# Kernel optimization log

Hardware: AMD Instinct MI355X
Metric: run time of the kernel (lower is better)

The kernel has to match this reference:

```python
import jax, jax.numpy as jnp
import numpy as np

N_NODES = 100000
N_EDGES = 3200000
IN_CH = 256
OUT_CH = 1


def setup_inputs() -> dict:
    key = jax.random.key(0)
    ks = jax.random.split(key, 8)
    x = jax.random.normal(ks[0], (N_NODES, IN_CH), dtype=jnp.float32)
    edge_index = jax.random.randint(ks[1], (2, N_EDGES), 0, N_NODES, dtype=jnp.int64 if jax.config.jax_enable_x64 else jnp.int32)
    s_in = 1.0 / np.sqrt(IN_CH)
    Wq = jax.random.uniform(ks[2], (IN_CH, OUT_CH), jnp.float32, -s_in, s_in)
    bq = jax.random.uniform(ks[3], (OUT_CH,), jnp.float32, -s_in, s_in)
    Wk = jax.random.uniform(ks[4], (IN_CH, OUT_CH), jnp.float32, -s_in, s_in)
    bk = jax.random.uniform(ks[5], (OUT_CH,), jnp.float32, -s_in, s_in)
    Wv = jax.random.uniform(ks[6], (IN_CH, IN_CH), jnp.float32, -s_in, s_in)
    bv = jax.random.uniform(ks[7], (IN_CH,), jnp.float32, -s_in, s_in)
    return {"x": x, "edge_index": edge_index, "Wq": Wq, "bq": bq,
            "Wk": Wk, "bk": bk, "Wv": Wv, "bv": bv}


def reference(x, edge_index, Wq, bq, Wk, bk, Wv, bv):
    num_nodes = x.shape[0]
    q = x @ Wq + bq                       # [N, out_ch]
    k = x @ Wk + bk                       # [N, out_ch]
    v = x @ Wv + bv                       # [N, in_ch]
    row, col = edge_index[0], edge_index[1]
    # edge attention logits: gather + dot over out_ch
    att = jnp.sum(q[row] * k[col], axis=-1)          # [E]
    att = jax.nn.leaky_relu(att, negative_slope=0.2)
    att = jax.nn.softmax(att, axis=0)                # softmax over ALL edges (dim=0)
    # scatter-add edge attention to source nodes
    attention_weights = jax.ops.segment_sum(att, row, num_segments=num_nodes)  # [N]
    graph_emb = jnp.sum(attention_weights[:, None] * v, axis=0)                # [in_ch]
    return graph_emb, attention_weights
```

## Files before the change

### kernel.cpp

```cpp
#include <hip/hip_runtime.h>

#define N_NODES 100000
#define N_EDGES 3200000
#define CH 256

#define EPB 2048
#define GS 1563
#define NB2 25
#define BSZ 4096
#define G_AGG 16
#define SLICE 98
#define GRID_QK 1563
#define GRID_POOL 512

#define OFF_TOTAL  0
#define OFF_PTOT   16
#define OFF_YUP    1584
#define OFF_PRE    132656
#define OFF_Q      173296
#define OFF_K      273296
#define OFF_PART   373296
#define OFF_EX     2011696
#define OFF_ROW    5212720

__global__ __launch_bounds__(256) void k_qk(const float* __restrict__ x,
                                            const float* __restrict__ Wq,
                                            const float* __restrict__ bq,
                                            const float* __restrict__ Wk,
                                            const float* __restrict__ bk,
                                            float* __restrict__ q,
                                            float* __restrict__ k) {
    int t = threadIdx.x;
    int w = t >> 6, lane = t & 63;
    int g = lane >> 4, seg = lane & 15;
    float4 wq4[4], wk4[4];
    #pragma unroll
    for (int j = 0; j < 4; ++j) {
        wq4[j] = ((const float4*)Wq)[seg + 16 * j];
        wk4[j] = ((const float4*)Wk)[seg + 16 * j];
    }
    float bqs = bq[0], bks = bk[0];
    int base = blockIdx.x * 64 + w * 16 + g;
    #pragma unroll
    for (int i = 0; i < 4; ++i) {
        int n = base + i * 4;
        if (n < N_NODES) {
            const float4* xr = (const float4*)(x + (size_t)n * CH);
            float dq = 0.0f, dk = 0.0f;
            #pragma unroll
            for (int j = 0; j < 4; ++j) {
                float4 xv = xr[seg + 16 * j];
                dq = fmaf(xv.x, wq4[j].x, fmaf(xv.y, wq4[j].y,
                     fmaf(xv.z, wq4[j].z, fmaf(xv.w, wq4[j].w, dq))));
                dk = fmaf(xv.x, wk4[j].x, fmaf(xv.y, wk4[j].y,
                     fmaf(xv.z, wk4[j].z, fmaf(xv.w, wk4[j].w, dk))));
            }
            dq += __shfl_down(dq, 8); dq += __shfl_down(dq, 4);
            dq += __shfl_down(dq, 2); dq += __shfl_down(dq, 1);
            dk += __shfl_down(dk, 8); dk += __shfl_down(dk, 4);
            dk += __shfl_down(dk, 2); dk += __shfl_down(dk, 1);
            if (seg == 0) { q[n] = dq + bqs; k[n] = dk + bks; }
        }
    }
}

__global__ __launch_bounds__(256) void k_sort(const int* __restrict__ ei,
                                              const float* __restrict__ q,
                                              const float* __restrict__ k,
                                              float* __restrict__ ex_out,
                                              unsigned short* __restrict__ row_out,
                                              int* __restrict__ pre,
                                              float* __restrict__ ptot) {
    __shared__ int cnt[4][NB2];
    __shared__ int bsum[NB2];
    __shared__ int pref[NB2 + 1];
    __shared__ float lex[EPB];
    __shared__ unsigned short lrow[EPB];
    __shared__ float sm[4];
    int t = threadIdx.x, blk = blockIdx.x, w = t >> 6;
    int e0 = blk * EPB;
    int ecnt = min(EPB, N_EDGES - e0);
    if (t < 4 * NB2) ((int*)cnt)[t] = 0;
    __syncthreads();
    int rr[8]; float ee[8];
    #pragma unroll
    for (int j = 0; j < 8; ++j) {
        int i = j * 256 + t;
        if (i < ecnt) {
            int r = ei[e0 + i], c = ei[N_EDGES + e0 + i];
            float v = q[r] * k[c];
            v = (v >= 0.0f) ? v : 0.2f * v;
            rr[j] = r; ee[j] = __expf(v);
            atomicAdd(&cnt[w][r >> 12], 1);
        } else { rr[j] = -1; ee[j] = 0.0f; }
    }
    __syncthreads();
    if (t < NB2) {
        int c0 = cnt[0][t], c1 = cnt[1][t], c2 = cnt[2][t], c3 = cnt[3][t];
        cnt[0][t] = 0; cnt[1][t] = c0; cnt[2][t] = c0 + c1; cnt[3][t] = c0 + c1 + c2;
        bsum[t] = c0 + c1 + c2 + c3;
    }
    __syncthreads();
    if (t == 0) {
        int run = 0;
        #pragma unroll
        for (int b = 0; b < NB2; ++b) { pref[b] = run; run += bsum[b]; }
        pref[NB2] = run;
    }
    __syncthreads();
    if (t < 4 * NB2) { int ww = t / NB2, b = t - ww * NB2; cnt[ww][b] += pref[b]; }
    if (t < NB2 + 1) pre[blk * 26 + t] = pref[t];
    __syncthreads();
    #pragma unroll
    for (int j = 0; j < 8; ++j) {
        if (rr[j] >= 0) {
            int b = rr[j] >> 12;
            int p = atomicAdd(&cnt[w][b], 1);
            lex[p] = ee[j];
            lrow[p] = (unsigned short)(rr[j] & (BSZ - 1));
        }
    }
    float s = ((ee[0] + ee[1]) + (ee[2] + ee[3])) + ((ee[4] + ee[5]) + (ee[6] + ee[7]));
    #pragma unroll
    for (int off = 32; off; off >>= 1) s += __shfl_down(s, off);
    if ((t & 63) == 0) sm[w] = s;
    __syncthreads();
    if (t == 0) ptot[blk] = sm[0] + sm[1] + sm[2] + sm[3];
    size_t gb = (size_t)blk * EPB;
    for (int i = t; i < ecnt; i += 256) ex_out[gb + i] = lex[i];
    unsigned* ro = (unsigned*)(row_out + gb);
    const unsigned* lr = (const unsigned*)lrow;
    int words = (ecnt + 1) >> 1;
    for (int i = t; i < words; i += 256) ro[i] = lr[i];
}

__global__ __launch_bounds__(256) void k_agg(const float* __restrict__ ex,
                                             const unsigned short* __restrict__ row,
                                             const int* __restrict__ pre,
                                             float* __restrict__ partial) {
    int b = blockIdx.x / G_AGG, g = blockIdx.x % G_AGG;
    __shared__ float acc[BSZ];
    int t = threadIdx.x, w = t >> 6, lane = t & 63;
    for (int i = t; i < BSZ; i += 256) acc[i] = 0.0f;
    __syncthreads();
    int sb0 = g * SLICE, sb1 = min(sb0 + SLICE, GS);
    for (int sb = sb0 + w; sb < sb1; sb += 4) {
        size_t gbase = (size_t)sb * EPB;
        int s0 = pre[sb * 26 + b], s1 = pre[sb * 26 + b + 1];
        for (int i = s0 + lane; i < s1; i += 64)
            atomicAdd(&acc[row[gbase + i]], ex[gbase + i]);
    }
    __syncthreads();
    float* dst = partial + ((size_t)b * G_AGG + g) * BSZ;
    for (int i = t; i < BSZ; i += 256) dst[i] = acc[i];
}

__global__ __launch_bounds__(256) void k_pool(const float* __restrict__ x,
                                              const float* __restrict__ partial,
                                              const float* __restrict__ ptot,
                                              float* __restrict__ totalp,
                                              float* __restrict__ yup,
                                              float* __restrict__ aw_out) {
    int t = threadIdx.x, s = t >> 6, g = t & 63;
    float ts = 0.0f;
    for (int i = t; i < GS; i += 256) ts += ptot[i];
    #pragma unroll
    for (int off = 32; off; off >>= 1) ts += __shfl_down(ts, off);
    __shared__ float sm[4];
    __shared__ float totsh;
    if (g == 0) sm[s] = ts;
    __syncthreads();
    if (t == 0) {
        totsh = sm[0] + sm[1] + sm[2] + sm[3];
        if (blockIdx.x == 0) totalp[0] = totsh;
    }
    __syncthreads();
    float inv = 1.0f / totsh;

    __shared__ float awA[2][8], awB[2][8];
    const float4* X4 = (const float4*)x;
    float4 acc = make_float4(0.f, 0.f, 0.f, 0.f);
    int p = 0;
    for (int base = blockIdx.x * 8; base < N_NODES; base += GRID_POOL * 8, p ^= 1) {
        int bkt = base >> 12, off = base & (BSZ - 1);
        float pv = 0.0f;
        if (t < 128) {
            int sl = t >> 3, no = t & 7;
            pv = partial[((size_t)bkt * G_AGG + sl) * BSZ + off + no];
        }
        pv += __shfl_down(pv, 32);
        pv += __shfl_down(pv, 16);
        pv += __shfl_down(pv, 8);
        if (t < 8) awA[p][t] = pv;
        else if (t >= 64 && t < 72) awB[p][t - 64] = pv;
        __syncthreads();
        float a0 = awA[p][s] + awB[p][s];
        float a1 = awA[p][4 + s] + awB[p][4 + s];
        if (t < 8) aw_out[base + t] = (awA[p][t] + awB[p][t]) * inv;
        float4 x0 = X4[(size_t)(base + s) * 64 + g];
        float4 x1 = X4[(size_t)(base + 4 + s) * 64 + g];
        acc.x = fmaf(a0, x0.x, acc.x); acc.y = fmaf(a0, x0.y, acc.y);
        acc.z = fmaf(a0, x0.z, acc.z); acc.w = fmaf(a0, x0.w, acc.w);
        acc.x = fmaf(a1, x1.x, acc.x); acc.y = fmaf(a1, x1.y, acc.y);
        acc.z = fmaf(a1, x1.z, acc.z); acc.w = fmaf(a1, x1.w, acc.w);
    }
    __syncthreads();
    __shared__ float4 tmp4[4][64];
    tmp4[s][g] = acc;
    __syncthreads();
    const float* tmp = (const float*)tmp4;
    float sum = tmp[0 * 256 + t] + tmp[1 * 256 + t] + tmp[2 * 256 + t] + tmp[3 * 256 + t];
    yup[(size_t)blockIdx.x * 256 + t] = sum;
}

__global__ __launch_bounds__(256) void k_final(const float* __restrict__ yup,
                                               const float* __restrict__ totalp,
                                               const float* __restrict__ Wv,
                                               const float* __restrict__ bv,
                                               float* __restrict__ out) {
    __shared__ float ysh[256];
    __shared__ float red[256];
    int t = threadIdx.x;
    float inv = 1.0f / totalp[0];
    float yv = 0.0f;
    #pragma unroll 8
    for (int r = 0; r < GRID_POOL; ++r) yv += yup[(size_t)r * 256 + t];
    ysh[t] = yv * inv;
    __syncthreads();
    int c = blockIdx.x * 32 + (t & 31), rg = t >> 5;
    float acc = 0.0f;
    #pragma unroll
    for (int j = 0; j < 32; ++j) {
        int kk = rg * 32 + j;
        acc = fmaf(ysh[kk], Wv[(size_t)kk * CH + c], acc);
    }
    red[t] = acc;
    __syncthreads();
    if (t < 32) {
        float sv = 0.0f;
        #pragma unroll
        for (int j = 0; j < 8; ++j) sv += red[j * 32 + t];
        out[blockIdx.x * 32 + t] = sv + bv[blockIdx.x * 32 + t];
    }
}

extern "C" void kernel_launch(void* const* d_in, const int* in_sizes, int n_in,
                              void* d_out, int out_size, void* d_ws, size_t ws_size,
                              hipStream_t stream) {
    const float* x  = (const float*)d_in[0];
    const int*   ei = (const int*)d_in[1];
    const float* Wq = (const float*)d_in[2];
    const float* bq = (const float*)d_in[3];
    const float* Wk = (const float*)d_in[4];
    const float* bk = (const float*)d_in[5];
    const float* Wv = (const float*)d_in[6];
    const float* bv = (const float*)d_in[7];
    float* out = (float*)d_out;
    float* ws  = (float*)d_ws;

    float*          totalp  = ws + OFF_TOTAL;
    float*          ptot    = ws + OFF_PTOT;
    float*          yup     = ws + OFF_YUP;
    int*            pre     = (int*)(ws + OFF_PRE);
    float*          q       = ws + OFF_Q;
    float*          k       = ws + OFF_K;
    float*          partial = ws + OFF_PART;
    float*          ex      = ws + OFF_EX;
    unsigned short* row     = (unsigned short*)(ws + OFF_ROW);

    hipLaunchKernelGGL(k_qk, dim3(GRID_QK), dim3(256), 0, stream,
                       x, Wq, bq, Wk, bk, q, k);
    hipLaunchKernelGGL(k_sort, dim3(GS), dim3(256), 0, stream,
                       ei, q, k, ex, row, pre, ptot);
    hipLaunchKernelGGL(k_agg, dim3(NB2 * G_AGG), dim3(256), 0, stream,
                       ex, row, pre, partial);
    hipLaunchKernelGGL(k_pool, dim3(GRID_POOL), dim3(256), 0, stream,
                       x, partial, ptot, totalp, yup, out + CH);
    hipLaunchKernelGGL(k_final, dim3(8), dim3(256), 0, stream,
                       yup, totalp, Wv, bv, out);
}
```

Baseline: 295.5 us.

## Split aggregation into more slices and move partial fold into separate kernel

After: 303.3 us. 2.6% more time.

```diff
diff --git a/kernel.cpp b/kernel.cpp
--- a/kernel.cpp
+++ b/kernel.cpp
@@ -8,20 +8,21 @@
 #define GS 1563
 #define NB2 25
 #define BSZ 4096
-#define G_AGG 16
-#define SLICE 98
+#define G_AGG 64
+#define SLICE 25
 #define GRID_QK 1563
 #define GRID_POOL 512
-
-#define OFF_TOTAL  0
+#define GRID_FOLD 391
+
 #define OFF_PTOT   16
 #define OFF_YUP    1584
 #define OFF_PRE    132656
 #define OFF_Q      173296
 #define OFF_K      273296
-#define OFF_PART   373296
-#define OFF_EX     2011696
-#define OFF_ROW    5212720
+#define OFF_AWU    373296
+#define OFF_PART   473296
+#define OFF_EX     7026896
+#define OFF_ROW    10227920
 
 __global__ __launch_bounds__(256) void k_qk(const float* __restrict__ x,
                                             const float* __restrict__ Wq,
@@ -138,16 +139,22 @@
                                              const unsigned short* __restrict__ row,
                                              const int* __restrict__ pre,
                                              float* __restrict__ partial) {
-    int b = blockIdx.x / G_AGG, g = blockIdx.x % G_AGG;
+    int b = blockIdx.x >> 6, g = blockIdx.x & 63;
     __shared__ float acc[BSZ];
-    int t = threadIdx.x, w = t >> 6, lane = t & 63;
+    __shared__ int segA[SLICE], segB[SLICE];
+    int t = threadIdx.x, hw = t >> 5, lane = t & 31;
     for (int i = t; i < BSZ; i += 256) acc[i] = 0.0f;
-    __syncthreads();
     int sb0 = g * SLICE, sb1 = min(sb0 + SLICE, GS);
-    for (int sb = sb0 + w; sb < sb1; sb += 4) {
-        size_t gbase = (size_t)sb * EPB;
-        int s0 = pre[sb * 26 + b], s1 = pre[sb * 26 + b + 1];
-        for (int i = s0 + lane; i < s1; i += 64)
+    int nseg = sb1 - sb0; if (nseg < 0) nseg = 0;
+    if (t < nseg) {
+        segA[t] = pre[(sb0 + t) * 26 + b];
+        segB[t] = pre[(sb0 + t) * 26 + b + 1];
+    }
+    __syncthreads();
+    for (int sI = hw; sI < nseg; sI += 8) {
+        size_t gbase = (size_t)(sb0 + sI) * EPB;
+        int s0 = segA[sI], s1 = segB[sI];
+        for (int i = s0 + lane; i < s1; i += 32)
             atomicAdd(&acc[row[gbase + i]], ex[gbase + i]);
     }
     __syncthreads();
@@ -155,48 +162,43 @@
     for (int i = t; i < BSZ; i += 256) dst[i] = acc[i];
 }
 
-__global__ __launch_bounds__(256) void k_pool(const float* __restrict__ x,
-                                              const float* __restrict__ partial,
+__global__ __launch_bounds__(256) void k_fold(const float* __restrict__ partial,
                                               const float* __restrict__ ptot,
-                                              float* __restrict__ totalp,
-                                              float* __restrict__ yup,
+                                              float* __restrict__ awu,
                                               float* __restrict__ aw_out) {
-    int t = threadIdx.x, s = t >> 6, g = t & 63;
+    int t = threadIdx.x;
     float ts = 0.0f;
     for (int i = t; i < GS; i += 256) ts += ptot[i];
     #pragma unroll
     for (int off = 32; off; off >>= 1) ts += __shfl_down(ts, off);
     __shared__ float sm[4];
     __shared__ float totsh;
-    if (g == 0) sm[s] = ts;
-    __syncthreads();
-    if (t == 0) {
-        totsh = sm[0] + sm[1] + sm[2] + sm[3];
-        if (blockIdx.x == 0) totalp[0] = totsh;
-    }
+    if ((t & 63) == 0) sm[t >> 6] = ts;
+    __syncthreads();
+    if (t == 0) totsh = sm[0] + sm[1] + sm[2] + sm[3];
     __syncthreads();
     float inv = 1.0f / totsh;
-
-    __shared__ float awA[2][8], awB[2][8];
+    int n = blockIdx.x * 256 + t;
+    if (n < N_NODES) {
+        int b = n >> 12, off = n & (BSZ - 1);
+        const float* p = partial + (size_t)b * G_AGG * BSZ + off;
+        float s = 0.0f;
+        #pragma unroll
+        for (int g = 0; g < G_AGG; ++g) s += p[(size_t)g * BSZ];
+        awu[n] = s;
+        aw_out[n] = s * inv;
+    }
+}
+
+__global__ __launch_bounds__(256) void k_pool(const float* __restrict__ x,
+                                              const float* __restrict__ awu,
+                                              float* __restrict__ yup) {
+    int t = threadIdx.x, s = t >> 6, g = t & 63;
     const float4* X4 = (const float4*)x;
     float4 acc = make_float4(0.f, 0.f, 0.f, 0.f);
-    int p = 0;
-    for (int base = blockIdx.x * 8; base < N_NODES; base += GRID_POOL * 8, p ^= 1) {
-        int bkt = base >> 12, off = base & (BSZ - 1);
-        float pv = 0.0f;
-        if (t < 128) {
-            int sl = t >> 3, no = t & 7;
-            pv = partial[((size_t)bkt * G_AGG + sl) * BSZ + off + no];
-        }
-        pv += __shfl_down(pv, 32);
-        pv += __shfl_down(pv, 16);
-        pv += __shfl_down(pv, 8);
-        if (t < 8) awA[p][t] = pv;
-        else if (t >= 64 && t < 72) awB[p][t - 64] = pv;
-        __syncthreads();
-        float a0 = awA[p][s] + awB[p][s];
-        float a1 = awA[p][4 + s] + awB[p][4 + s];
-        if (t < 8) aw_out[base + t] = (awA[p][t] + awB[p][t]) * inv;
+    for (int base = blockIdx.x * 8; base < N_NODES; base += GRID_POOL * 8) {
+        float a0 = awu[base + s];
+        float a1 = awu[base + 4 + s];
         float4 x0 = X4[(size_t)(base + s) * 64 + g];
         float4 x1 = X4[(size_t)(base + 4 + s) * 64 + g];
         acc.x = fmaf(a0, x0.x, acc.x); acc.y = fmaf(a0, x0.y, acc.y);
@@ -204,7 +206,6 @@
         acc.x = fmaf(a1, x1.x, acc.x); acc.y = fmaf(a1, x1.y, acc.y);
         acc.z = fmaf(a1, x1.z, acc.z); acc.w = fmaf(a1, x1.w, acc.w);
     }
-    __syncthreads();
     __shared__ float4 tmp4[4][64];
     tmp4[s][g] = acc;
     __syncthreads();
@@ -214,14 +215,24 @@
 }
 
 __global__ __launch_bounds__(256) void k_final(const float* __restrict__ yup,
-                                               const float* __restrict__ totalp,
+                                               const float* __restrict__ ptot,
                                                const float* __restrict__ Wv,
                                                const float* __restrict__ bv,
                                                float* __restrict__ out) {
     __shared__ float ysh[256];
     __shared__ float red[256];
+    __shared__ float sm[4];
+    __shared__ float totsh;
     int t = threadIdx.x;
-    float inv = 1.0f / totalp[0];
+    float ts = 0.0f;
+    for (int i = t; i < GS; i += 256) ts += ptot[i];
+    #pragma unroll
+    for (int off = 32; off; off >>= 1) ts += __shfl_down(ts, off);
+    if ((t & 63) == 0) sm[t >> 6] = ts;
+    __syncthreads();
+    if (t == 0) totsh = sm[0] + sm[1] + sm[2] + sm[3];
+    __syncthreads();
+    float inv = 1.0f / totsh;
     float yv = 0.0f;
     #pragma unroll 8
     for (int r = 0; r < GRID_POOL; ++r) yv += yup[(size_t)r * 256 + t];
@@ -258,12 +269,12 @@
     float* out = (float*)d_out;
     float* ws  = (float*)d_ws;
 
-    float*          totalp  = ws + OFF_TOTAL;
     float*          ptot    = ws + OFF_PTOT;
     float*          yup     = ws + OFF_YUP;
     int*            pre     = (int*)(ws + OFF_PRE);
     float*          q       = ws + OFF_Q;
     float*          k       = ws + OFF_K;
+    float*          awu     = ws + OFF_AWU;
     float*          partial = ws + OFF_PART;
     float*          ex      = ws + OFF_EX;
     unsigned short* row     = (unsigned short*)(ws + OFF_ROW);
@@ -274,8 +285,10 @@
                        ei, q, k, ex, row, pre, ptot);
     hipLaunchKernelGGL(k_agg, dim3(NB2 * G_AGG), dim3(256), 0, stream,
                        ex, row, pre, partial);
+    hipLaunchKernelGGL(k_fold, dim3(GRID_FOLD), dim3(256), 0, stream,
+                       partial, ptot, awu, out + CH);
     hipLaunchKernelGGL(k_pool, dim3(GRID_POOL), dim3(256), 0, stream,
-                       x, partial, ptot, totalp, yup, out + CH);
+                       x, awu, yup);
     hipLaunchKernelGGL(k_final, dim3(8), dim3(256), 0, stream,
-                       yup, totalp, Wv, bv, out);
-}
+                       yup, ptot, Wv, bv, out);
+}
```

## Fuse all stages into one persistent kernel with software grid barriers

Applied to the files above, without the earlier changes.

Result: slower. 621.5 us (+110.3%).

```diff
diff --git a/kernel.cpp b/kernel.cpp
--- a/kernel.cpp
+++ b/kernel.cpp
@@ -4,243 +4,287 @@
 #define N_EDGES 3200000
 #define CH 256
 
-#define EPB 2048
-#define GS 1563
+#define GRID_C 768
+#define EPB 2084
+#define TILES 1536
 #define NB2 25
 #define BSZ 4096
-#define G_AGG 16
-#define SLICE 98
-#define GRID_QK 1563
-#define GRID_POOL 512
-
-#define OFF_TOTAL  0
+#define G_AGG 30
+#define SLICE 52
+#define CHUNK 131
+
+#define OFF_BAR    0
 #define OFF_PTOT   16
-#define OFF_YUP    1584
-#define OFF_PRE    132656
-#define OFF_Q      173296
-#define OFF_K      273296
-#define OFF_PART   373296
-#define OFF_EX     2011696
-#define OFF_ROW    5212720
-
-__global__ __launch_bounds__(256) void k_qk(const float* __restrict__ x,
-                                            const float* __restrict__ Wq,
-                                            const float* __restrict__ bq,
-                                            const float* __restrict__ Wk,
-                                            const float* __restrict__ bk,
-                                            float* __restrict__ q,
-                                            float* __restrict__ k) {
-    int t = threadIdx.x;
-    int w = t >> 6, lane = t & 63;
-    int g = lane >> 4, seg = lane & 15;
-    float4 wq4[4], wk4[4];
-    #pragma unroll
-    for (int j = 0; j < 4; ++j) {
-        wq4[j] = ((const float4*)Wq)[seg + 16 * j];
-        wk4[j] = ((const float4*)Wk)[seg + 16 * j];
-    }
-    float bqs = bq[0], bks = bk[0];
-    int base = blockIdx.x * 64 + w * 16 + g;
-    #pragma unroll
-    for (int i = 0; i < 4; ++i) {
-        int n = base + i * 4;
-        if (n < N_NODES) {
-            const float4* xr = (const float4*)(x + (size_t)n * CH);
-            float dq = 0.0f, dk = 0.0f;
+#define OFF_YUP    1552
+#define OFF_PRE    198160
+#define OFF_Q      238096
+#define OFF_K      338096
+#define OFF_PART   438096
+#define OFF_EX     3510096
+#define OFF_ROW    6711120
+
+struct SMemSort {
+    int cnt[4][NB2];
+    int bsum[NB2];
+    int pref[NB2 + 1];
+    float sm[4];
+    float lex[EPB];
+    unsigned short lrow[EPB];
+};
+struct SMemAgg {
+    float acc[BSZ];
+    int segA[SLICE];
+    int segB[SLICE];
+};
+struct SMemPool {
+    float awn[CHUNK + 5];
+    float sm[4];
+    float totsh;
+    float4 tmp4[4][64];
+};
+struct SMemFin {
+    float ysh[256];
+    float red[256];
+};
+union SMemU {
+    SMemSort s;
+    SMemAgg a;
+    SMemPool p;
+    SMemFin f;
+};
+
+__device__ __forceinline__ void gridbar(int* bar, int slot, int nblk) {
+    __syncthreads();
+    if (threadIdx.x == 0) {
+        __threadfence();
+        atomicAdd(&bar[slot], 1);
+        while (__hip_atomic_load(&bar[slot], __ATOMIC_RELAXED,
+                                 __HIP_MEMORY_SCOPE_AGENT) < nblk)
+            __builtin_amdgcn_s_sleep(2);
+        __threadfence();
+    }
+    __syncthreads();
+}
+
+__global__ void k_binit(int* bar) {
+    if (threadIdx.x < 8) bar[threadIdx.x] = 0;
+}
+
+__global__ __launch_bounds__(256, 3) void k_fused(
+        const float* __restrict__ x, const int* __restrict__ ei,
+        const float* __restrict__ Wq, const float* __restrict__ bq,
+        const float* __restrict__ Wk, const float* __restrict__ bk,
+        const float* __restrict__ Wv, const float* __restrict__ bv,
+        float* __restrict__ out, float* __restrict__ ws) {
+    __shared__ SMemU sm;
+    int t = threadIdx.x, blk = blockIdx.x;
+
+    int*            bar     = (int*)ws;
+    float*          ptot    = ws + OFF_PTOT;
+    float*          yup     = ws + OFF_YUP;
+    int*            pre     = (int*)(ws + OFF_PRE);
+    float*          q       = ws + OFF_Q;
+    float*          k       = ws + OFF_K;
+    float*          partial = ws + OFF_PART;
+    float*          ex      = ws + OFF_EX;
+    unsigned short* row     = (unsigned short*)(ws + OFF_ROW);
+    float*          aw_out  = out + CH;
+
+    {
+        int w = t >> 6, lane = t & 63, g = lane >> 4, seg = lane & 15;
+        float4 wq4[4], wk4[4];
+        #pragma unroll
+        for (int j = 0; j < 4; ++j) {
+            wq4[j] = ((const float4*)Wq)[seg + 16 * j];
+            wk4[j] = ((const float4*)Wk)[seg + 16 * j];
+        }
+        float bqs = bq[0], bks = bk[0];
+        for (int b0 = blk * 64; b0 < N_NODES; b0 += GRID_C * 64) {
+            int base = b0 + w * 16 + g;
             #pragma unroll
-            for (int j = 0; j < 4; ++j) {
-                float4 xv = xr[seg + 16 * j];
-                dq = fmaf(xv.x, wq4[j].x, fmaf(xv.y, wq4[j].y,
-                     fmaf(xv.z, wq4[j].z, fmaf(xv.w, wq4[j].w, dq))));
-                dk = fmaf(xv.x, wk4[j].x, fmaf(xv.y, wk4[j].y,
-                     fmaf(xv.z, wk4[j].z, fmaf(xv.w, wk4[j].w, dk))));
+            for (int i = 0; i < 4; ++i) {
+                int n = base + i * 4;
+                if (n < N_NODES) {
+                    const float4* xr = (const float4*)(x + (size_t)n * CH);
+                    float dq = 0.0f, dk = 0.0f;
+                    #pragma unroll
+                    for (int j = 0; j < 4; ++j) {
+                        float4 xv = xr[seg + 16 * j];
+                        dq = fmaf(xv.x, wq4[j].x, fmaf(xv.y, wq4[j].y,
+                             fmaf(xv.z, wq4[j].z, fmaf(xv.w, wq4[j].w, dq))));
+                        dk = fmaf(xv.x, wk4[j].x, fmaf(xv.y, wk4[j].y,
+                             fmaf(xv.z, wk4[j].z, fmaf(xv.w, wk4[j].w, dk))));
+                    }
+                    dq += __shfl_down(dq, 8); dq += __shfl_down(dq, 4);
+                    dq += __shfl_down(dq, 2); dq += __shfl_down(dq, 1);
+                    dk += __shfl_down(dk, 8); dk += __shfl_down(dk, 4);
+                    dk += __shfl_down(dk, 2); dk += __shfl_down(dk, 1);
+                    if (seg == 0) { q[n] = dq + bqs; k[n] = dk + bks; }
+                }
             }
-            dq += __shfl_down(dq, 8); dq += __shfl_down(dq, 4);
-            dq += __shfl_down(dq, 2); dq += __shfl_down(dq, 1);
-            dk += __shfl_down(dk, 8); dk += __shfl_down(dk, 4);
-            dk += __shfl_down(dk, 2); dk += __shfl_down(dk, 1);
-            if (seg == 0) { q[n] = dq + bqs; k[n] = dk + bks; }
-        }
-    }
-}
-
-__global__ __launch_bounds__(256) void k_sort(const int* __restrict__ ei,
-                                              const float* __restrict__ q,
-                                              const float* __restrict__ k,
-                                              float* __restrict__ ex_out,
-                                              unsigned short* __restrict__ row_out,
-                                              int* __restrict__ pre,
-                                              float* __restrict__ ptot) {
-    __shared__ int cnt[4][NB2];
-    __shared__ int bsum[NB2];
-    __shared__ int pref[NB2 + 1];
-    __shared__ float lex[EPB];
-    __shared__ unsigned short lrow[EPB];
-    __shared__ float sm[4];
-    int t = threadIdx.x, blk = blockIdx.x, w = t >> 6;
-    int e0 = blk * EPB;
-    int ecnt = min(EPB, N_EDGES - e0);
-    if (t < 4 * NB2) ((int*)cnt)[t] = 0;
-    __syncthreads();
-    int rr[8]; float ee[8];
-    #pragma unroll
-    for (int j = 0; j < 8; ++j) {
-        int i = j * 256 + t;
-        if (i < ecnt) {
-            int r = ei[e0 + i], c = ei[N_EDGES + e0 + i];
-            float v = q[r] * k[c];
-            v = (v >= 0.0f) ? v : 0.2f * v;
-            rr[j] = r; ee[j] = __expf(v);
-            atomicAdd(&cnt[w][r >> 12], 1);
-        } else { rr[j] = -1; ee[j] = 0.0f; }
-    }
-    __syncthreads();
-    if (t < NB2) {
-        int c0 = cnt[0][t], c1 = cnt[1][t], c2 = cnt[2][t], c3 = cnt[3][t];
-        cnt[0][t] = 0; cnt[1][t] = c0; cnt[2][t] = c0 + c1; cnt[3][t] = c0 + c1 + c2;
-        bsum[t] = c0 + c1 + c2 + c3;
-    }
-    __syncthreads();
-    if (t == 0) {
-        int run = 0;
-        #pragma unroll
-        for (int b = 0; b < NB2; ++b) { pref[b] = run; run += bsum[b]; }
-        pref[NB2] = run;
-    }
-    __syncthreads();
-    if (t < 4 * NB2) { int ww = t / NB2, b = t - ww * NB2; cnt[ww][b] += pref[b]; }
-    if (t < NB2 + 1) pre[blk * 26 + t] = pref[t];
-    __syncthreads();
-    #pragma unroll
-    for (int j = 0; j < 8; ++j) {
-        if (rr[j] >= 0) {
-            int b = rr[j] >> 12;
-            int p = atomicAdd(&cnt[w][b], 1);
-            lex[p] = ee[j];
-            lrow[p] = (unsigned short)(rr[j] & (BSZ - 1));
-        }
-    }
-    float s = ((ee[0] + ee[1]) + (ee[2] + ee[3])) + ((ee[4] + ee[5]) + (ee[6] + ee[7]));
-    #pragma unroll
-    for (int off = 32; off; off >>= 1) s += __shfl_down(s, off);
-    if ((t & 63) == 0) sm[w] = s;
-    __syncthreads();
-    if (t == 0) ptot[blk] = sm[0] + sm[1] + sm[2] + sm[3];
-    size_t gb = (size_t)blk * EPB;
-    for (int i = t; i < ecnt; i += 256) ex_out[gb + i] = lex[i];
-    unsigned* ro = (unsigned*)(row_out + gb);
-    const unsigned* lr = (const unsigned*)lrow;
-    int words = (ecnt + 1) >> 1;
-    for (int i = t; i < words; i += 256) ro[i] = lr[i];
-}
-
-__global__ __launch_bounds__(256) void k_agg(const float* __restrict__ ex,
-                                             const unsigned short* __restrict__ row,
-                                             const int* __restrict__ pre,
-                                             float* __restrict__ partial) {
-    int b = blockIdx.x / G_AGG, g = blockIdx.x % G_AGG;
-    __shared__ float acc[BSZ];
-    int t = threadIdx.x, w = t >> 6, lane = t & 63;
-    for (int i = t; i < BSZ; i += 256) acc[i] = 0.0f;
-    __syncthreads();
-    int sb0 = g * SLICE, sb1 = min(sb0 + SLICE, GS);
-    for (int sb = sb0 + w; sb < sb1; sb += 4) {
-        size_t gbase = (size_t)sb * EPB;
-        int s0 = pre[sb * 26 + b], s1 = pre[sb * 26 + b + 1];
-        for (int i = s0 + lane; i < s1; i += 64)
-            atomicAdd(&acc[row[gbase + i]], ex[gbase + i]);
-    }
-    __syncthreads();
-    float* dst = partial + ((size_t)b * G_AGG + g) * BSZ;
-    for (int i = t; i < BSZ; i += 256) dst[i] = acc[i];
-}
-
-__global__ __launch_bounds__(256) void k_pool(const float* __restrict__ x,
-                                              const float* __restrict__ partial,
-                                              const float* __restrict__ ptot,
-                                              float* __restrict__ totalp,
-                                              float* __restrict__ yup,
-                                              float* __restrict__ aw_out) {
-    int t = threadIdx.x, s = t >> 6, g = t & 63;
-    float ts = 0.0f;
-    for (int i = t; i < GS; i += 256) ts += ptot[i];
-    #pragma unroll
-    for (int off = 32; off; off >>= 1) ts += __shfl_down(ts, off);
-    __shared__ float sm[4];
-    __shared__ float totsh;
-    if (g == 0) sm[s] = ts;
-    __syncthreads();
-    if (t == 0) {
-        totsh = sm[0] + sm[1] + sm[2] + sm[3];
-        if (blockIdx.x == 0) totalp[0] = totsh;
-    }
-    __syncthreads();
-    float inv = 1.0f / totsh;
-
-    __shared__ float awA[2][8], awB[2][8];
-    const float4* X4 = (const float4*)x;
-    float4 acc = make_float4(0.f, 0.f, 0.f, 0.f);
-    int p = 0;
-    for (int base = blockIdx.x * 8; base < N_NODES; base += GRID_POOL * 8, p ^= 1) {
-        int bkt = base >> 12, off = base & (BSZ - 1);
-        float pv = 0.0f;
-        if (t < 128) {
-            int sl = t >> 3, no = t & 7;
-            pv = partial[((size_t)bkt * G_AGG + sl) * BSZ + off + no];
-        }
-        pv += __shfl_down(pv, 32);
-        pv += __shfl_down(pv, 16);
-        pv += __shfl_down(pv, 8);
-        if (t < 8) awA[p][t] = pv;
-        else if (t >= 64 && t < 72) awB[p][t - 64] = pv;
-        __syncthreads();
-        float a0 = awA[p][s] + awB[p][s];
-        float a1 = awA[p][4 + s] + awB[p][4 + s];
-        if (t < 8) aw_out[base + t] = (awA[p][t] + awB[p][t]) * inv;
-        float4 x0 = X4[(size_t)(base + s) * 64 + g];
-        float4 x1 = X4[(size_t)(base + 4 + s) * 64 + g];
-        acc.x = fmaf(a0, x0.x, acc.x); acc.y = fmaf(a0, x0.y, acc.y);
-        acc.z = fmaf(a0, x0.z, acc.z); acc.w = fmaf(a0, x0.w, acc.w);
-        acc.x = fmaf(a1, x1.x, acc.x); acc.y = fmaf(a1, x1.y, acc.y);
-        acc.z = fmaf(a1, x1.z, acc.z); acc.w = fmaf(a1, x1.w, acc.w);
-    }
-    __syncthreads();
-    __shared__ float4 tmp4[4][64];
-    tmp4[s][g] = acc;
-    __syncthreads();
-    const float* tmp = (const float*)tmp4;
-    float sum = tmp[0 * 256 + t] + tmp[1 * 256 + t] + tmp[2 * 256 + t] + tmp[3 * 256 + t];
-    yup[(size_t)blockIdx.x * 256 + t] = sum;
-}
-
-__global__ __launch_bounds__(256) void k_final(const float* __restrict__ yup,
-                                               const float* __restrict__ totalp,
-                                               const float* __restrict__ Wv,
-                                               const float* __restrict__ bv,
-                                               float* __restrict__ out) {
-    __shared__ float ysh[256];
-    __shared__ float red[256];
-    int t = threadIdx.x;
-    float inv = 1.0f / totalp[0];
-    float yv = 0.0f;
-    #pragma unroll 8
-    for (int r = 0; r < GRID_POOL; ++r) yv += yup[(size_t)r * 256 + t];
-    ysh[t] = yv * inv;
-    __syncthreads();
-    int c = blockIdx.x * 32 + (t & 31), rg = t >> 5;
-    float acc = 0.0f;
-    #pragma unroll
-    for (int j = 0; j < 32; ++j) {
-        int kk = rg * 32 + j;
-        acc = fmaf(ysh[kk], Wv[(size_t)kk * CH + c], acc);
-    }
-    red[t] = acc;
-    __syncthreads();
-    if (t < 32) {
-        float sv = 0.0f;
-        #pragma unroll
-        for (int j = 0; j < 8; ++j) sv += red[j * 32 + t];
-        out[blockIdx.x * 32 + t] = sv + bv[blockIdx.x * 32 + t];
+        }
+    }
+    gridbar(bar, 0, GRID_C);
+
+    for (int tile = blk; tile < TILES; tile += GRID_C) {
+        int e0 = tile * EPB;
+        int ecnt = min(EPB, N_EDGES - e0);
+        int w = t >> 6;
+        if (t < 4 * NB2) ((int*)sm.s.cnt)[t] = 0;
+        __syncthreads();
+        int rr[9]; float ee[9];
+        #pragma unroll
+        for (int j = 0; j < 9; ++j) {
+            int i = j * 256 + t;
+            if (i < ecnt) {
+                int r = ei[e0 + i], c = ei[N_EDGES + e0 + i];
+                float v = q[r] * k[c];
+                v = (v >= 0.0f) ? v : 0.2f * v;
+                rr[j] = r; ee[j] = __expf(v);
+                atomicAdd(&sm.s.cnt[w][r >> 12], 1);
+            } else { rr[j] = -1; ee[j] = 0.0f; }
+        }
+        __syncthreads();
+        if (t < NB2) {
+            int c0 = sm.s.cnt[0][t], c1 = sm.s.cnt[1][t];
+            int c2 = sm.s.cnt[2][t], c3 = sm.s.cnt[3][t];
+            sm.s.cnt[0][t] = 0; sm.s.cnt[1][t] = c0;
+            sm.s.cnt[2][t] = c0 + c1; sm.s.cnt[3][t] = c0 + c1 + c2;
+            sm.s.bsum[t] = c0 + c1 + c2 + c3;
+        }
+        __syncthreads();
+        if (t == 0) {
+            int run = 0;
+            #pragma unroll
+            for (int b = 0; b < NB2; ++b) { sm.s.pref[b] = run; run += sm.s.bsum[b]; }
+            sm.s.pref[NB2] = run;
+        }
+        __syncthreads();
+        if (t < 4 * NB2) {
+            int ww = t / NB2, b = t - ww * NB2;
+            sm.s.cnt[ww][b] += sm.s.pref[b];
+        }
+        if (t < NB2 + 1) pre[tile * 26 + t] = sm.s.pref[t];
+        __syncthreads();
+        #pragma unroll
+        for (int j = 0; j < 9; ++j) {
+            if (rr[j] >= 0) {
+                int b = rr[j] >> 12;
+                int p = atomicAdd(&sm.s.cnt[w][b], 1);
+                sm.s.lex[p] = ee[j];
+                sm.s.lrow[p] = (unsigned short)(rr[j] & (BSZ - 1));
+            }
+        }
+        float s = 0.0f;
+        #pragma unroll
+        for (int j = 0; j < 9; ++j) s += ee[j];
+        #pragma unroll
+        for (int off = 32; off; off >>= 1) s += __shfl_down(s, off);
+        if ((t & 63) == 0) sm.s.sm[w] = s;
+        __syncthreads();
+        if (t == 0) ptot[tile] = sm.s.sm[0] + sm.s.sm[1] + sm.s.sm[2] + sm.s.sm[3];
+        size_t gb = (size_t)tile * EPB;
+        for (int i = t; i < ecnt; i += 256) ex[gb + i] = sm.s.lex[i];
+        unsigned* ro = (unsigned*)(row + gb);
+        const unsigned* lr = (const unsigned*)sm.s.lrow;
+        int words = (ecnt + 1) >> 1;
+        for (int i = t; i < words; i += 256) ro[i] = lr[i];
+    }
+    gridbar(bar, 1, GRID_C);
+
+    if (blk < NB2 * G_AGG) {
+        int b = blk / G_AGG, g = blk % G_AGG;
+        for (int i = t; i < BSZ; i += 256) sm.a.acc[i] = 0.0f;
+        int sb0 = g * SLICE, sb1 = min(sb0 + SLICE, TILES);
+        int nseg = sb1 - sb0;
+        if (t < nseg) {
+            sm.a.segA[t] = pre[(sb0 + t) * 26 + b];
+            sm.a.segB[t] = pre[(sb0 + t) * 26 + b + 1];
+        }
+        __syncthreads();
+        int hw = t >> 5, lane = t & 31;
+        for (int sI = hw; sI < nseg; sI += 8) {
+            size_t gb = (size_t)(sb0 + sI) * EPB;
+            int s0 = sm.a.segA[sI], s1 = sm.a.segB[sI];
+            for (int i = s0 + lane; i < s1; i += 32)
+                atomicAdd(&sm.a.acc[row[gb + i]], ex[gb + i]);
+        }
+        __syncthreads();
+        float* dst = partial + ((size_t)b * G_AGG + g) * BSZ;
+        for (int i = t; i < BSZ; i += 256) dst[i] = sm.a.acc[i];
+    }
+    gridbar(bar, 2, GRID_C);
+
+    {
+        float ts = 0.0f;
+        for (int i = t; i < TILES; i += 256) ts += ptot[i];
+        #pragma unroll
+        for (int off = 32; off; off >>= 1) ts += __shfl_down(ts, off);
+        if ((t & 63) == 0) sm.p.sm[t >> 6] = ts;
+        __syncthreads();
+        if (t == 0) sm.p.totsh = sm.p.sm[0] + sm.p.sm[1] + sm.p.sm[2] + sm.p.sm[3];
+        __syncthreads();
+        float inv = 1.0f / sm.p.totsh;
+        int n0 = blk * CHUNK;
+        int cnt = min(CHUNK, N_NODES - n0);
+        if (t < cnt) {
+            int n = n0 + t, bb = n >> 12, off = n & (BSZ - 1);
+            const float* p = partial + (size_t)bb * G_AGG * BSZ + off;
+            float ssum = 0.0f;
+            #pragma unroll 10
+            for (int g = 0; g < G_AGG; ++g) ssum += p[(size_t)g * BSZ];
+            float an = ssum * inv;
+            sm.p.awn[t] = an;
+            aw_out[n] = an;
+        }
+        __syncthreads();
+        int s4 = t >> 6, g4 = t & 63;
+        const float4* X4 = (const float4*)x;
+        float4 acc = make_float4(0.f, 0.f, 0.f, 0.f);
+        for (int i0 = 0; i0 < cnt; i0 += 8) {
+            int i1 = i0 + s4, i2 = i0 + 4 + s4;
+            if (i1 < cnt) {
+                float a0 = sm.p.awn[i1];
+                float4 x0 = X4[(size_t)(n0 + i1) * 64 + g4];
+                acc.x = fmaf(a0, x0.x, acc.x); acc.y = fmaf(a0, x0.y, acc.y);
+                acc.z = fmaf(a0, x0.z, acc.z); acc.w = fmaf(a0, x0.w, acc.w);
+            }
+            if (i2 < cnt) {
+                float a1 = sm.p.awn[i2];
+                float4 x1 = X4[(size_t)(n0 + i2) * 64 + g4];
+                acc.x = fmaf(a1, x1.x, acc.x); acc.y = fmaf(a1, x1.y, acc.y);
+                acc.z = fmaf(a1, x1.z, acc.z); acc.w = fmaf(a1, x1.w, acc.w);
+            }
+        }
+        sm.p.tmp4[s4][g4] = acc;
+        __syncthreads();
+        const float* tmp = (const float*)sm.p.tmp4;
+        float sum = tmp[0 * 256 + t] + tmp[1 * 256 + t] + tmp[2 * 256 + t] + tmp[3 * 256 + t];
+        yup[(size_t)blk * 256 + t] = sum;
+    }
+    gridbar(bar, 3, GRID_C);
+
+    if (blk < 8) {
+        float yv = 0.0f;
+        #pragma unroll 8
+        for (int r = 0; r < GRID_C; ++r) yv += yup[(size_t)r * 256 + t];
+        sm.f.ysh[t] = yv;
+        __syncthreads();
+        int c = blk * 32 + (t & 31), rg = t >> 5;
+        float acc = 0.0f;
+        #pragma unroll
+        for (int j = 0; j < 32; ++j) {
+            int kk = rg * 32 + j;
+            acc = fmaf(sm.f.ysh[kk], Wv[(size_t)kk * CH + c], acc);
+        }
+        sm.f.red[t] = acc;
+        __syncthreads();
+        if (t < 32) {
+            float sv = 0.0f;
+            #pragma unroll
+            for (int j = 0; j < 8; ++j) sv += sm.f.red[j * 32 + t];
+            out[blk * 32 + t] = sv + bv[blk * 32 + t];
+        }
     }
 }
 
@@ -258,24 +302,7 @@
     float* out = (float*)d_out;
     float* ws  = (float*)d_ws;
 
-    float*          totalp  = ws + OFF_TOTAL;
-    float*          ptot    = ws + OFF_PTOT;
-    float*          yup     = ws + OFF_YUP;
-    int*            pre     = (int*)(ws + OFF_PRE);
-    float*          q       = ws + OFF_Q;
-    float*          k       = ws + OFF_K;
-    float*          partial = ws + OFF_PART;
-    float*          ex      = ws + OFF_EX;
-    unsigned short* row     = (unsigned short*)(ws + OFF_ROW);
-
-    hipLaunchKernelGGL(k_qk, dim3(GRID_QK), dim3(256), 0, stream,
-                       x, Wq, bq, Wk, bk, q, k);
-    hipLaunchKernelGGL(k_sort, dim3(GS), dim3(256), 0, stream,
-                       ei, q, k, ex, row, pre, ptot);
-    hipLaunchKernelGGL(k_agg, dim3(NB2 * G_AGG), dim3(256), 0, stream,
-                       ex, row, pre, partial);
-    hipLaunchKernelGGL(k_pool, dim3(GRID_POOL), dim3(256), 0, stream,
-                       x, partial, ptot, totalp, yup, out + CH);
-    hipLaunchKernelGGL(k_final, dim3(8), dim3(256), 0, stream,
-                       yup, totalp, Wv, bv, out);
+    hipLaunchKernelGGL(k_binit, dim3(1), dim3(64), 0, stream, (int*)ws);
+    hipLaunchKernelGGL(k_fused, dim3(GRID_C), dim3(256), 0, stream,
+                       x, ei, Wq, bq, Wk, bk, Wv, bv, out, ws);
 }
```
